# Kernel optimization log

Measured on AMD Instinct MI355X. Metric: run time of the kernel, lower is better.

## Reference

```python
import jax, jax.numpy as jnp
import numpy as np

S, B, QD, VD, E = 2048, 32, 1024, 1024, 1024


def setup_inputs() -> dict:
    key = jax.random.key(0)
    ks = jax.random.split(key, 8)
    query = jax.random.normal(ks[0], (B, QD), dtype=jnp.float32)
    value = jax.random.normal(ks[1], (S, B, VD), dtype=jnp.float32)
    key_padding_mask = jnp.zeros((S, B), dtype=bool)
    # learned params, init as in reset_parameters()
    Wq = jax.random.uniform(ks[2], (E, QD), minval=-0.1, maxval=0.1, dtype=jnp.float32)
    Wv = jax.random.uniform(ks[3], (E, VD), minval=-0.1, maxval=0.1, dtype=jnp.float32)
    v = jax.random.uniform(ks[4], (E,), minval=-0.1, maxval=0.1, dtype=jnp.float32)
    b = jnp.zeros((E,), dtype=jnp.float32)
    g = jnp.full((1,), float(np.sqrt(1.0 / E)), dtype=jnp.float32)
    return {"query": query, "value": value, "Wq": Wq, "Wv": Wv, "v": v, "b": b, "g": g,
            "key_padding_mask": key_padding_mask}


def reference(query, value, Wq, Wv, v, b, g, key_padding_mask):
    # projected_query: (B, E) -> broadcast over seq dim
    pq = query @ Wq.T
    # key: (S, B, E)
    key = jnp.einsum('sbd,ed->sbe', value, Wv)
    normed_v = g * v / jnp.linalg.norm(v)  # (E,)
    # additive (Bahdanau) scores: (S, B)
    attn_scores = jnp.einsum('e,sbe->sb', normed_v, jnp.tanh(pq[None, :, :] + key + b))
    attn_scores = jnp.where(key_padding_mask, -jnp.inf, attn_scores)
    attn_scores = jax.nn.softmax(attn_scores, axis=0)  # softmax over seq dim
    context = jnp.einsum('sb,sbd->bd', attn_scores, value)  # (B, VD)
    return (context, attn_scores, attn_scores)
```

## Files before the change

kernel.cpp:

```cpp
#include <hip/hip_runtime.h>
#include <hip/hip_bf16.h>
#include <stdint.h>

#define SEQ 2048
#define BAT 32
#define EDIM 1024
#define MROWS (SEQ*BAT)

typedef __bf16 bf16x8 __attribute__((ext_vector_type(8)));
typedef float f32x4 __attribute__((ext_vector_type(4)));
typedef unsigned short u16x8 __attribute__((ext_vector_type(8)));

typedef __attribute__((address_space(3))) unsigned int lds_uint;
typedef const __attribute__((address_space(1))) unsigned int glb_uint;

__device__ __forceinline__ void async16(void* lds, const void* g) {
  __builtin_amdgcn_global_load_lds((glb_uint*)g, (lds_uint*)lds, 16, 0, 0);
}

__device__ __forceinline__ unsigned short f2bf(float f) {
  unsigned u = __builtin_bit_cast(unsigned, f);
  u = (u + 0x7FFFu + ((u >> 16) & 1u)) >> 16;
  return (unsigned short)u;
}
__device__ __forceinline__ float bf2f(unsigned short h) {
  return __builtin_bit_cast(float, (unsigned)h << 16);
}

__device__ __forceinline__ float fast_tanh(float x) {
  float xc = fminf(fmaxf(x, -9.f), 9.f);
  float e = __expf(2.f * xc);
  return (e - 1.f) * __builtin_amdgcn_rcpf(e + 1.f);
}

__global__ void k_nv(const float* __restrict__ v, const float* __restrict__ g,
                     float* __restrict__ nv) {
  __shared__ float red[256];
  int t = threadIdx.x;
  float s = 0.f;
  for (int i = t; i < EDIM; i += 256) { float x = v[i]; s += x * x; }
  red[t] = s; __syncthreads();
  for (int o = 128; o > 0; o >>= 1) {
    if (t < o) red[t] += red[t + o];
    __syncthreads();
  }
  float scale = g[0] / sqrtf(red[0]);
  for (int i = t; i < EDIM; i += 256) nv[i] = v[i] * scale;
}

__global__ void k_pqb(const float* __restrict__ query, const float* __restrict__ Wq,
                      const float* __restrict__ bias, float* __restrict__ pqb) {
  __shared__ float wq[1024];
  int e = blockIdx.x;
  int t = threadIdx.x;
  reinterpret_cast<float4*>(wq)[t] =
      reinterpret_cast<const float4*>(Wq + (size_t)e * EDIM)[t];
  __syncthreads();
  int w = t >> 6, lane = t & 63;
  float be = bias[e];
  for (int bb = 0; bb < 8; ++bb) {
    int b_ = w * 8 + bb;
    const float4* q4 = reinterpret_cast<const float4*>(query + (size_t)b_ * EDIM) + lane * 4;
    const float4* w4 = reinterpret_cast<const float4*>(wq) + lane * 4;
    float s = 0.f;
#pragma unroll
    for (int j = 0; j < 4; ++j) {
      float4 a = q4[j], c = w4[j];
      s += a.x * c.x + a.y * c.y + a.z * c.z + a.w * c.w;
    }
#pragma unroll
    for (int m = 32; m > 0; m >>= 1) s += __shfl_xor(s, m);
    if (lane == 0) pqb[(size_t)b_ * EDIM + e] = s + be;
  }
}

__global__ void k_cvt(const float* __restrict__ in, unsigned short* __restrict__ out,
                      long long n8) {
  long long i = (long long)blockIdx.x * blockDim.x + threadIdx.x;
  long long stride = (long long)gridDim.x * blockDim.x;
  for (; i < n8; i += stride) {
    const float4* p = reinterpret_cast<const float4*>(in + i * 8);
    float4 a = p[0], b = p[1];
    u16x8 r;
    r[0] = f2bf(a.x); r[1] = f2bf(a.y); r[2] = f2bf(a.z); r[3] = f2bf(a.w);
    r[4] = f2bf(b.x); r[5] = f2bf(b.y); r[6] = f2bf(b.z); r[7] = f2bf(b.w);
    *reinterpret_cast<u16x8*>(out + i * 8) = r;
  }
}

__global__ __launch_bounds__(512, 1) void k_gemm(
    const unsigned short* __restrict__ A,
    const unsigned short* __restrict__ Bm,
    const float* __restrict__ pqb,
    const float* __restrict__ nv,
    float* __restrict__ part)
{
  __shared__ char smem[2 * 65536 + 4 * 256 * 4];

  const int tid = threadIdx.x;
  const int lane = tid & 63;
  const int wid = tid >> 6;
  const int wm = wid >> 2;
  const int wn = wid & 3;

  const int bid = blockIdx.x;
  const int x = bid & 7;
  const int j = bid >> 3;
  const int mi_blk = x * 32 + (j >> 2);
  const int ni_blk = j & 3;
  const size_t m0 = (size_t)mi_blk * 256;
  const int n0 = ni_blk * 256;

  float* partLds = (float*)(smem + 131072);

  f32x4 acc[8][4];
#pragma unroll
  for (int i = 0; i < 8; ++i)
#pragma unroll
    for (int jj = 0; jj < 4; ++jj) acc[i][jj] = f32x4{0.f, 0.f, 0.f, 0.f};

  const int cs0 = (lane >> 4) ^ (lane & 7);
  const int cs1 = cs0 ^ 4;
  const int rA = lane & 15;

  auto stageA = [&](int slot, int k0) {
#pragma unroll
    for (int i = 0; i < 4; ++i) {
      int chunk = i * 512 + tid;
      int row = chunk >> 3;
      int csrc = (chunk & 7) ^ (row & 7);
      async16(smem + slot * 65536 + chunk * 16,
              A + (m0 + (size_t)row) * 1024 + k0 + csrc * 8);
    }
  };
  auto stageB = [&](int slot, int k0) {
#pragma unroll
    for (int i = 0; i < 4; ++i) {
      int chunk = i * 512 + tid;
      int row = chunk >> 3;
      int csrc = (chunk & 7) ^ (row & 7);
      async16(smem + slot * 65536 + 32768 + chunk * 16,
              Bm + (size_t)(n0 + row) * 1024 + k0 + csrc * 8);
    }
  };

  stageA(0, 0);
  stageB(0, 0);
  __syncthreads();

#pragma unroll 1
  for (int t = 0; t < 16; ++t) {
    char* cb = smem + (t & 1) * 65536;
    const int nslot = (t + 1) & 1;
    const int nk0 = (t + 1) * 64;
    const bool pf = (t + 1) < 16;

    if (pf) stageA(nslot, nk0);

#pragma unroll
    for (int kk = 0; kk < 2; ++kk) {
      const int cs = kk ? cs1 : cs0;
      bf16x8 af[8], bf[4];
#pragma unroll
      for (int mi = 0; mi < 8; ++mi)
        af[mi] = *reinterpret_cast<const bf16x8*>(
            cb + (wm * 128 + mi * 16 + rA) * 128 + cs * 16);
#pragma unroll
      for (int nj = 0; nj < 2; ++nj)
        bf[nj] = *reinterpret_cast<const bf16x8*>(
            cb + 32768 + (wn * 64 + nj * 16 + rA) * 128 + cs * 16);

      __builtin_amdgcn_s_setprio(1);
#pragma unroll
      for (int mi = 0; mi < 8; ++mi)
#pragma unroll
        for (int nj = 0; nj < 2; ++nj)
          acc[mi][nj] = __builtin_amdgcn_mfma_f32_16x16x32_bf16(af[mi], bf[nj], acc[mi][nj], 0, 0, 0);
      __builtin_amdgcn_s_setprio(0);

      if (kk == 0 && pf) stageB(nslot, nk0);

#pragma unroll
      for (int nj = 2; nj < 4; ++nj)
        bf[nj] = *reinterpret_cast<const bf16x8*>(
            cb + 32768 + (wn * 64 + nj * 16 + rA) * 128 + cs * 16);

      __builtin_amdgcn_s_setprio(1);
#pragma unroll
      for (int mi = 0; mi < 8; ++mi)
#pragma unroll
        for (int nj = 2; nj < 4; ++nj)
          acc[mi][nj] = __builtin_amdgcn_mfma_f32_16x16x32_bf16(af[mi], bf[nj], acc[mi][nj], 0, 0, 0);
      __builtin_amdgcn_s_setprio(0);
    }
    __syncthreads();
  }

  const int cgrp = lane >> 4;
  const int ccol = lane & 15;
  float nve[4];
#pragma unroll
  for (int nj = 0; nj < 4; ++nj) nve[nj] = nv[n0 + wn * 64 + nj * 16 + ccol];

#pragma unroll
  for (int mi = 0; mi < 8; ++mi) {
#pragma unroll
    for (int r = 0; r < 4; ++r) {
      int rloc = wm * 128 + mi * 16 + cgrp * 4 + r;
      int b_ = rloc & 31;
      const float* pq = pqb + (size_t)b_ * EDIM + n0 + wn * 64 + ccol;
      float s = 0.f;
#pragma unroll
      for (int nj = 0; nj < 4; ++nj)
        s += nve[nj] * fast_tanh(acc[mi][nj][r] + pq[nj * 16]);
      s += __shfl_xor(s, 1);
      s += __shfl_xor(s, 2);
      s += __shfl_xor(s, 4);
      s += __shfl_xor(s, 8);
      if (ccol == 0) partLds[wn * 256 + rloc] = s;
    }
  }
  __syncthreads();
  if (tid < 256)
    part[(size_t)ni_blk * MROWS + m0 + tid] =
        partLds[tid] + partLds[256 + tid] + partLds[512 + tid] + partLds[768 + tid];
}

__global__ void k_softmax(const float* __restrict__ part,
                          const unsigned char* __restrict__ mask,
                          float* __restrict__ scores,
                          float* __restrict__ out_attn)
{
  int b_ = blockIdx.x;
  int t = threadIdx.x;
  __shared__ float red[256];
  float sc[8];
  float mx = -1e30f;
#pragma unroll
  for (int i = 0; i < 8; ++i) {
    int s_ = t + i * 256;
    size_t r = (size_t)s_ * BAT + b_;
    float v = 0.f;
#pragma unroll
    for (int c = 0; c < 4; ++c) v += part[(size_t)c * MROWS + r];
    if (mask[r]) v = -1e30f;
    sc[i] = v;
    mx = fmaxf(mx, v);
  }
  red[t] = mx; __syncthreads();
  for (int o = 128; o > 0; o >>= 1) {
    if (t < o) red[t] = fmaxf(red[t], red[t + o]);
    __syncthreads();
  }
  mx = red[0];
  __syncthreads();
  float sum = 0.f;
#pragma unroll
  for (int i = 0; i < 8; ++i) { sc[i] = expf(sc[i] - mx); sum += sc[i]; }
  red[t] = sum; __syncthreads();
  for (int o = 128; o > 0; o >>= 1) {
    if (t < o) red[t] += red[t + o];
    __syncthreads();
  }
  float inv = 1.f / red[0];
#pragma unroll
  for (int i = 0; i < 8; ++i) {
    int s_ = t + i * 256;
    size_t r = (size_t)s_ * BAT + b_;
    float w = sc[i] * inv;
    scores[r] = w;
    out_attn[r] = w;
    out_attn[MROWS + r] = w;
  }
}

__global__ void k_ctx(const unsigned short* __restrict__ Vb,
                      const float* __restrict__ scores,
                      float* __restrict__ pctx)
{
  int b_ = blockIdx.x;
  int sch = blockIdx.y;
  int t = threadIdx.x;
  int d8 = t & 127;
  int sr = t >> 7;
  float acc[8];
#pragma unroll
  for (int j = 0; j < 8; ++j) acc[j] = 0.f;
  int s0 = sch * 256;
  for (int i = 0; i < 128; ++i) {
    int s_ = s0 + i * 2 + sr;
    size_t r = (size_t)s_ * BAT + b_;
    float w = scores[r];
    u16x8 v = *reinterpret_cast<const u16x8*>(Vb + r * 1024 + d8 * 8);
#pragma unroll
    for (int j = 0; j < 8; ++j) acc[j] += w * bf2f(v[j]);
  }
  float* dst = pctx + ((size_t)(sch * 2 + sr) * BAT + b_) * 1024 + d8 * 8;
#pragma unroll
  for (int j = 0; j < 8; ++j) dst[j] = acc[j];
}

__global__ void k_ctx_reduce(const float* __restrict__ pctx, float* __restrict__ out) {
  int i = blockIdx.x * 256 + threadIdx.x;
  float s = 0.f;
#pragma unroll
  for (int c = 0; c < 16; ++c) s += pctx[(size_t)c * 32768 + i];
  out[i] = s;
}

extern "C" void kernel_launch(void* const* d_in, const int* in_sizes, int n_in,
                              void* d_out, int out_size, void* d_ws, size_t ws_size,
                              hipStream_t stream) {
  const float* query = (const float*)d_in[0];
  const float* value = (const float*)d_in[1];
  const float* Wq    = (const float*)d_in[2];
  const float* Wv    = (const float*)d_in[3];
  const float* v     = (const float*)d_in[4];
  const float* bias  = (const float*)d_in[5];
  const float* g     = (const float*)d_in[6];
  const unsigned char* mask = (const unsigned char*)d_in[7];
  float* out = (float*)d_out;

  char* ws = (char*)d_ws;
  unsigned short* Vb  = (unsigned short*)ws;
  unsigned short* Wvb = (unsigned short*)(ws + (size_t)134217728);
  float* pqb    = (float*)(ws + (size_t)134217728 + 2097152);
  float* nv     = pqb + 32 * 1024;
  float* part   = nv + 1024;
  float* scores = part + 4 * MROWS;
  float* pctx   = scores + MROWS;

  k_nv<<<1, 256, 0, stream>>>(v, g, nv);
  k_pqb<<<1024, 256, 0, stream>>>(query, Wq, bias, pqb);
  k_cvt<<<2048, 256, 0, stream>>>(value, Vb, (long long)(65536LL * 1024 / 8));
  k_cvt<<<512, 256, 0, stream>>>(Wv, Wvb, (long long)(1024LL * 1024 / 8));
  k_gemm<<<1024, 512, 0, stream>>>(Vb, Wvb, pqb, nv, part);
  k_softmax<<<32, 256, 0, stream>>>(part, mask, scores, out + 32768);
  dim3 gf(32, 8);
  k_ctx<<<gf, 256, 0, stream>>>(Vb, scores, pctx);
  k_ctx_reduce<<<128, 256, 0, stream>>>(pctx, out);
}
```

Before: 273.7 us.

## Switch GEMM to 32x32x16 MFMA with precomputed pointers and unrolled double buffer

Replaces the 16x16x32 bf16 MFMA tiling with 32x32x16 MFMA, so each wave issues 8 larger MFMAs per k-step instead of 32 small ones and needs fewer LDS fragment reads per flop. Global-load addresses are precomputed once and bumped each iteration, and the double-buffer loop is manually unrolled by two to drop per-iteration slot arithmetic. The epilogue is rewritten for the 32x32 accumulator layout with an extra shuffle step. This risks different register pressure and a changed LDS bank-conflict pattern under the new swizzle.

```diff
diff --git a/kernel.cpp b/kernel.cpp
--- a/kernel.cpp
+++ b/kernel.cpp
@@ -8,7 +8,7 @@
 #define MROWS (SEQ*BAT)
 
 typedef __bf16 bf16x8 __attribute__((ext_vector_type(8)));
-typedef float f32x4 __attribute__((ext_vector_type(4)));
+typedef float f32x16 __attribute__((ext_vector_type(16)));
 typedef unsigned short u16x8 __attribute__((ext_vector_type(8)));
 
 typedef __attribute__((address_space(3))) unsigned int lds_uint;
@@ -102,122 +102,116 @@
   const int wid = tid >> 6;
   const int wm = wid >> 2;
   const int wn = wid & 3;
+  const int l31 = lane & 31;
+  const int hi = lane >> 5;
 
   const int bid = blockIdx.x;
-  const int x = bid & 7;
+  const int xcd = bid & 7;
   const int j = bid >> 3;
-  const int mi_blk = x * 32 + (j >> 2);
+  const int mi_blk = xcd * 32 + (j >> 2);
   const int ni_blk = j & 3;
   const size_t m0 = (size_t)mi_blk * 256;
   const int n0 = ni_blk * 256;
 
   float* partLds = (float*)(smem + 131072);
 
-  f32x4 acc[8][4];
-#pragma unroll
-  for (int i = 0; i < 8; ++i)
-#pragma unroll
-    for (int jj = 0; jj < 4; ++jj) acc[i][jj] = f32x4{0.f, 0.f, 0.f, 0.f};
-
-  const int cs0 = (lane >> 4) ^ (lane & 7);
-  const int cs1 = cs0 ^ 4;
-  const int rA = lane & 15;
-
-  auto stageA = [&](int slot, int k0) {
-#pragma unroll
-    for (int i = 0; i < 4; ++i) {
-      int chunk = i * 512 + tid;
-      int row = chunk >> 3;
-      int csrc = (chunk & 7) ^ (row & 7);
-      async16(smem + slot * 65536 + chunk * 16,
-              A + (m0 + (size_t)row) * 1024 + k0 + csrc * 8);
-    }
+  f32x16 acc[4][2];
+#pragma unroll
+  for (int i = 0; i < 4; ++i)
+#pragma unroll
+    for (int jj = 0; jj < 2; ++jj) acc[i][jj] = (f32x16)(0.f);
+
+  const int csrc = (tid & 7) ^ ((tid >> 3) & 7);
+  const unsigned short* gA[4];
+  const unsigned short* gB[4];
+#pragma unroll
+  for (int i = 0; i < 4; ++i) {
+    int row = i * 64 + (tid >> 3);
+    gA[i] = A + (m0 + (size_t)row) * 1024 + csrc * 8;
+    gB[i] = Bm + (size_t)(n0 + row) * 1024 + csrc * 8;
+  }
+  const int ldsOffA = tid * 16;
+  const int ldsOffB = 32768 + tid * 16;
+
+  const int swz = ((hi ^ (lane & 7)) << 4);
+  const int rdA = (wm * 128 + l31) * 128 + swz;
+  const int rdB = 32768 + (wn * 64 + l31) * 128 + swz;
+
+  auto stageA = [&](char* sl) {
+#pragma unroll
+    for (int i = 0; i < 4; ++i)
+      async16(sl + ldsOffA + i * 8192, gA[i]);
   };
-  auto stageB = [&](int slot, int k0) {
-#pragma unroll
-    for (int i = 0; i < 4; ++i) {
-      int chunk = i * 512 + tid;
-      int row = chunk >> 3;
-      int csrc = (chunk & 7) ^ (row & 7);
-      async16(smem + slot * 65536 + 32768 + chunk * 16,
-              Bm + (size_t)(n0 + row) * 1024 + k0 + csrc * 8);
-    }
+  auto stageB = [&](char* sl) {
+#pragma unroll
+    for (int i = 0; i < 4; ++i)
+      async16(sl + ldsOffB + i * 8192, gB[i]);
   };
-
-  stageA(0, 0);
-  stageB(0, 0);
+  auto bump = [&]() {
+#pragma unroll
+    for (int i = 0; i < 4; ++i) { gA[i] += 64; gB[i] += 64; }
+  };
+
+  char* buf0 = smem;
+  char* buf1 = smem + 65536;
+
+  stageA(buf0);
+  stageB(buf0);
+  bump();
   __syncthreads();
 
-#pragma unroll 1
-  for (int t = 0; t < 16; ++t) {
-    char* cb = smem + (t & 1) * 65536;
-    const int nslot = (t + 1) & 1;
-    const int nk0 = (t + 1) * 64;
-    const bool pf = (t + 1) < 16;
-
-    if (pf) stageA(nslot, nk0);
-
-#pragma unroll
-    for (int kk = 0; kk < 2; ++kk) {
-      const int cs = kk ? cs1 : cs0;
-      bf16x8 af[8], bf[4];
-#pragma unroll
-      for (int mi = 0; mi < 8; ++mi)
-        af[mi] = *reinterpret_cast<const bf16x8*>(
-            cb + (wm * 128 + mi * 16 + rA) * 128 + cs * 16);
-#pragma unroll
-      for (int nj = 0; nj < 2; ++nj)
-        bf[nj] = *reinterpret_cast<const bf16x8*>(
-            cb + 32768 + (wn * 64 + nj * 16 + rA) * 128 + cs * 16);
+  auto body = [&](char* cb, char* nb, bool pf) {
+    if (pf) stageA(nb);
+#pragma unroll
+    for (int ks = 0; ks < 4; ++ks) {
+      const int x = ks << 5;
+      bf16x8 af[4], bf[2];
+#pragma unroll
+      for (int fm = 0; fm < 4; ++fm)
+        af[fm] = *reinterpret_cast<const bf16x8*>(cb + ((rdA ^ x) + fm * 4096));
+#pragma unroll
+      for (int fn = 0; fn < 2; ++fn)
+        bf[fn] = *reinterpret_cast<const bf16x8*>(cb + ((rdB ^ x) + fn * 4096));
+
+      if (ks == 1 && pf) stageB(nb);
 
       __builtin_amdgcn_s_setprio(1);
 #pragma unroll
-      for (int mi = 0; mi < 8; ++mi)
-#pragma unroll
-        for (int nj = 0; nj < 2; ++nj)
-          acc[mi][nj] = __builtin_amdgcn_mfma_f32_16x16x32_bf16(af[mi], bf[nj], acc[mi][nj], 0, 0, 0);
-      __builtin_amdgcn_s_setprio(0);
-
-      if (kk == 0 && pf) stageB(nslot, nk0);
-
-#pragma unroll
-      for (int nj = 2; nj < 4; ++nj)
-        bf[nj] = *reinterpret_cast<const bf16x8*>(
-            cb + 32768 + (wn * 64 + nj * 16 + rA) * 128 + cs * 16);
-
-      __builtin_amdgcn_s_setprio(1);
-#pragma unroll
-      for (int mi = 0; mi < 8; ++mi)
-#pragma unroll
-        for (int nj = 2; nj < 4; ++nj)
-          acc[mi][nj] = __builtin_amdgcn_mfma_f32_16x16x32_bf16(af[mi], bf[nj], acc[mi][nj], 0, 0, 0);
+      for (int fm = 0; fm < 4; ++fm)
+#pragma unroll
+        for (int fn = 0; fn < 2; ++fn)
+          acc[fm][fn] = __builtin_amdgcn_mfma_f32_32x32x16_bf16(af[fm], bf[fn], acc[fm][fn], 0, 0, 0);
       __builtin_amdgcn_s_setprio(0);
     }
+    if (pf) bump();
     __syncthreads();
-  }
-
-  const int cgrp = lane >> 4;
-  const int ccol = lane & 15;
-  float nve[4];
-#pragma unroll
-  for (int nj = 0; nj < 4; ++nj) nve[nj] = nv[n0 + wn * 64 + nj * 16 + ccol];
-
-#pragma unroll
-  for (int mi = 0; mi < 8; ++mi) {
-#pragma unroll
-    for (int r = 0; r < 4; ++r) {
-      int rloc = wm * 128 + mi * 16 + cgrp * 4 + r;
-      int b_ = rloc & 31;
-      const float* pq = pqb + (size_t)b_ * EDIM + n0 + wn * 64 + ccol;
-      float s = 0.f;
-#pragma unroll
-      for (int nj = 0; nj < 4; ++nj)
-        s += nve[nj] * fast_tanh(acc[mi][nj][r] + pq[nj * 16]);
+  };
+
+#pragma unroll 1
+  for (int tt = 0; tt < 8; ++tt) {
+    body(buf0, buf1, true);
+    body(buf1, buf0, tt < 7);
+  }
+
+  float nve[2];
+#pragma unroll
+  for (int fn = 0; fn < 2; ++fn) nve[fn] = nv[n0 + wn * 64 + fn * 32 + l31];
+
+#pragma unroll
+  for (int fm = 0; fm < 4; ++fm) {
+#pragma unroll
+    for (int r = 0; r < 16; ++r) {
+      int b_ = (r & 3) + 8 * (r >> 2) + 4 * hi;
+      int m_loc = wm * 128 + fm * 32 + b_;
+      const float* pq = pqb + (size_t)b_ * EDIM + n0 + wn * 64 + l31;
+      float s = nve[0] * fast_tanh(acc[fm][0][r] + pq[0]) +
+                nve[1] * fast_tanh(acc[fm][1][r] + pq[32]);
       s += __shfl_xor(s, 1);
       s += __shfl_xor(s, 2);
       s += __shfl_xor(s, 4);
       s += __shfl_xor(s, 8);
-      if (ccol == 0) partLds[wn * 256 + rloc] = s;
+      s += __shfl_xor(s, 16);
+      if (l31 == 0) partLds[wn * 256 + m_loc] = s;
     }
   }
   __syncthreads();
```

After: 309.9 us. +13.2%, slower.

## Restructure GEMM mainloop into 4-stage K=32 pipeline with vmcnt waits

Applied to the files above, without the earlier changes.

Replaces the double-buffered K=64 tile loop with a four-slot ring of K=32 tiles, prefetching three stages ahead. Each step uses one barrier plus explicit s_waitcnt vmcnt counts instead of a full __syncthreads after every tile. The LDS swizzle is reworked for 64-byte rows. The aim is to hide global-load latency better and cut synchronisation stalls. In exchange it has twice as many barriers per K, and correctness now depends on hand-picked vmcnt values and buffer reuse ordering.

```diff
diff --git a/kernel.cpp b/kernel.cpp
--- a/kernel.cpp
+++ b/kernel.cpp
@@ -13,6 +13,8 @@
 
 typedef __attribute__((address_space(3))) unsigned int lds_uint;
 typedef const __attribute__((address_space(1))) unsigned int glb_uint;
+
+#define WAITV(n) asm volatile("s_waitcnt vmcnt(" #n ")" ::: "memory")
 
 __device__ __forceinline__ void async16(void* lds, const void* g) {
   __builtin_amdgcn_global_load_lds((glb_uint*)g, (lds_uint*)lds, 16, 0, 0);
@@ -95,7 +97,7 @@
     const float* __restrict__ nv,
     float* __restrict__ part)
 {
-  __shared__ char smem[2 * 65536 + 4 * 256 * 4];
+  __shared__ char smem[4 * 32768 + 4 * 256 * 4];
 
   const int tid = threadIdx.x;
   const int lane = tid & 63;
@@ -104,9 +106,9 @@
   const int wn = wid & 3;
 
   const int bid = blockIdx.x;
-  const int x = bid & 7;
+  const int xcd = bid & 7;
   const int j = bid >> 3;
-  const int mi_blk = x * 32 + (j >> 2);
+  const int mi_blk = xcd * 32 + (j >> 2);
   const int ni_blk = j & 3;
   const size_t m0 = (size_t)mi_blk * 256;
   const int n0 = ni_blk * 256;
@@ -119,88 +121,70 @@
 #pragma unroll
     for (int jj = 0; jj < 4; ++jj) acc[i][jj] = f32x4{0.f, 0.f, 0.f, 0.f};
 
-  const int cs0 = (lane >> 4) ^ (lane & 7);
-  const int cs1 = cs0 ^ 4;
+  const int csrc = (tid & 3) ^ ((tid >> 2) & 3);
+  const int row0 = tid >> 2;
+  const unsigned short* gA0 = A + (m0 + (size_t)row0) * 1024 + csrc * 8;
+  const unsigned short* gA1 = gA0 + 128 * 1024;
+  const unsigned short* gB0 = Bm + (size_t)(n0 + row0) * 1024 + csrc * 8;
+  const unsigned short* gB1 = gB0 + 128 * 1024;
+  const int dst0 = tid * 16;
+
+  auto stage = [&](char* buf) {
+    async16(buf + dst0, gA0);
+    async16(buf + 8192 + dst0, gA1);
+    async16(buf + 16384 + dst0, gB0);
+    async16(buf + 24576 + dst0, gB1);
+    gA0 += 32; gA1 += 32; gB0 += 32; gB1 += 32;
+  };
+
   const int rA = lane & 15;
-
-  auto stageA = [&](int slot, int k0) {
-#pragma unroll
-    for (int i = 0; i < 4; ++i) {
-      int chunk = i * 512 + tid;
-      int row = chunk >> 3;
-      int csrc = (chunk & 7) ^ (row & 7);
-      async16(smem + slot * 65536 + chunk * 16,
-              A + (m0 + (size_t)row) * 1024 + k0 + csrc * 8);
-    }
+  const int swz = (((lane >> 4) ^ (lane & 3)) << 4);
+  const int rdA = (wm * 128 + rA) * 64 + swz;
+  const int rdB = 16384 + (wn * 64 + rA) * 64 + swz;
+
+  auto half_step = [&](char* cb, char* sb) {
+    __builtin_amdgcn_s_barrier();
+    if (sb) stage(sb);
+    bf16x8 af[8], bf[4];
+#pragma unroll
+    for (int mi = 0; mi < 8; ++mi)
+      af[mi] = *reinterpret_cast<const bf16x8*>(cb + rdA + mi * 1024);
+#pragma unroll
+    for (int fn = 0; fn < 4; ++fn)
+      bf[fn] = *reinterpret_cast<const bf16x8*>(cb + rdB + fn * 1024);
+    __builtin_amdgcn_s_setprio(1);
+#pragma unroll
+    for (int mi = 0; mi < 8; ++mi)
+#pragma unroll
+      for (int fn = 0; fn < 4; ++fn)
+        acc[mi][fn] = __builtin_amdgcn_mfma_f32_16x16x32_bf16(af[mi], bf[fn], acc[mi][fn], 0, 0, 0);
+    __builtin_amdgcn_s_setprio(0);
   };
-  auto stageB = [&](int slot, int k0) {
-#pragma unroll
-    for (int i = 0; i < 4; ++i) {
-      int chunk = i * 512 + tid;
-      int row = chunk >> 3;
-      int csrc = (chunk & 7) ^ (row & 7);
-      async16(smem + slot * 65536 + 32768 + chunk * 16,
-              Bm + (size_t)(n0 + row) * 1024 + k0 + csrc * 8);
-    }
-  };
-
-  stageA(0, 0);
-  stageB(0, 0);
-  __syncthreads();
+
+  char* b0 = smem;
+  char* b1 = smem + 32768;
+  char* b2 = smem + 65536;
+  char* b3 = smem + 98304;
+
+  stage(b0); stage(b1); stage(b2);
 
 #pragma unroll 1
-  for (int t = 0; t < 16; ++t) {
-    char* cb = smem + (t & 1) * 65536;
-    const int nslot = (t + 1) & 1;
-    const int nk0 = (t + 1) * 64;
-    const bool pf = (t + 1) < 16;
-
-    if (pf) stageA(nslot, nk0);
-
-#pragma unroll
-    for (int kk = 0; kk < 2; ++kk) {
-      const int cs = kk ? cs1 : cs0;
-      bf16x8 af[8], bf[4];
-#pragma unroll
-      for (int mi = 0; mi < 8; ++mi)
-        af[mi] = *reinterpret_cast<const bf16x8*>(
-            cb + (wm * 128 + mi * 16 + rA) * 128 + cs * 16);
-#pragma unroll
-      for (int nj = 0; nj < 2; ++nj)
-        bf[nj] = *reinterpret_cast<const bf16x8*>(
-            cb + 32768 + (wn * 64 + nj * 16 + rA) * 128 + cs * 16);
-
-      __builtin_amdgcn_s_setprio(1);
-#pragma unroll
-      for (int mi = 0; mi < 8; ++mi)
-#pragma unroll
-        for (int nj = 0; nj < 2; ++nj)
-          acc[mi][nj] = __builtin_amdgcn_mfma_f32_16x16x32_bf16(af[mi], bf[nj], acc[mi][nj], 0, 0, 0);
-      __builtin_amdgcn_s_setprio(0);
-
-      if (kk == 0 && pf) stageB(nslot, nk0);
-
-#pragma unroll
-      for (int nj = 2; nj < 4; ++nj)
-        bf[nj] = *reinterpret_cast<const bf16x8*>(
-            cb + 32768 + (wn * 64 + nj * 16 + rA) * 128 + cs * 16);
-
-      __builtin_amdgcn_s_setprio(1);
-#pragma unroll
-      for (int mi = 0; mi < 8; ++mi)
-#pragma unroll
-        for (int nj = 2; nj < 4; ++nj)
-          acc[mi][nj] = __builtin_amdgcn_mfma_f32_16x16x32_bf16(af[mi], bf[nj], acc[mi][nj], 0, 0, 0);
-      __builtin_amdgcn_s_setprio(0);
-    }
-    __syncthreads();
-  }
+  for (int it = 0; it < 7; ++it) {
+    WAITV(8); half_step(b0, b3);
+    WAITV(8); half_step(b1, b0);
+    WAITV(8); half_step(b2, b1);
+    WAITV(8); half_step(b3, b2);
+  }
+  WAITV(8); half_step(b0, b3);
+  WAITV(8); half_step(b1, nullptr);
+  WAITV(4); half_step(b2, nullptr);
+  WAITV(0); half_step(b3, nullptr);
 
   const int cgrp = lane >> 4;
   const int ccol = lane & 15;
   float nve[4];
 #pragma unroll
-  for (int nj = 0; nj < 4; ++nj) nve[nj] = nv[n0 + wn * 64 + nj * 16 + ccol];
+  for (int fn = 0; fn < 4; ++fn) nve[fn] = nv[n0 + wn * 64 + fn * 16 + ccol];
 
 #pragma unroll
   for (int mi = 0; mi < 8; ++mi) {
@@ -211,8 +195,8 @@
       const float* pq = pqb + (size_t)b_ * EDIM + n0 + wn * 64 + ccol;
       float s = 0.f;
 #pragma unroll
-      for (int nj = 0; nj < 4; ++nj)
-        s += nve[nj] * fast_tanh(acc[mi][nj][r] + pq[nj * 16]);
+      for (int fn = 0; fn < 4; ++fn)
+        s += nve[fn] * fast_tanh(acc[mi][fn][r] + pq[fn * 16]);
       s += __shfl_xor(s, 1);
       s += __shfl_xor(s, 2);
       s += __shfl_xor(s, 4);
```

New measurement: 286.4 us. 4.6% more time.

## Fuse fp32-to-bf16 conversion of value into GEMM A-tile loading

Applied to the files above, without the earlier changes.

Removes the separate conversion kernel over the large value tensor. The GEMM now loads fp32 value rows into registers, converts them to bf16 and writes them to LDS. Blocks in the first N-tile column also write the bf16 copy to global memory for the later context kernel. This saves one full read and write pass of the 256MB tensor, but each of the four N-blocks per row tile now reads the fp32 A data (twice the bytes of bf16) instead of using async global-to-LDS loads, which adds register pressure and synchronous load latency. Conversion also switches to the compiler's native bf16 cast instead of manual rounding.

```diff
diff --git a/kernel.cpp b/kernel.cpp
--- a/kernel.cpp
+++ b/kernel.cpp
@@ -25,6 +25,13 @@
 }
 __device__ __forceinline__ float bf2f(unsigned short h) {
   return __builtin_bit_cast(float, (unsigned)h << 16);
+}
+
+__device__ __forceinline__ u16x8 cvt8(float4 a, float4 b) {
+  bf16x8 r;
+  r[0] = (__bf16)a.x; r[1] = (__bf16)a.y; r[2] = (__bf16)a.z; r[3] = (__bf16)a.w;
+  r[4] = (__bf16)b.x; r[5] = (__bf16)b.y; r[6] = (__bf16)b.z; r[7] = (__bf16)b.w;
+  return __builtin_bit_cast(u16x8, r);
 }
 
 __device__ __forceinline__ float fast_tanh(float x) {
@@ -81,18 +88,16 @@
   for (; i < n8; i += stride) {
     const float4* p = reinterpret_cast<const float4*>(in + i * 8);
     float4 a = p[0], b = p[1];
-    u16x8 r;
-    r[0] = f2bf(a.x); r[1] = f2bf(a.y); r[2] = f2bf(a.z); r[3] = f2bf(a.w);
-    r[4] = f2bf(b.x); r[5] = f2bf(b.y); r[6] = f2bf(b.z); r[7] = f2bf(b.w);
-    *reinterpret_cast<u16x8*>(out + i * 8) = r;
+    *reinterpret_cast<u16x8*>(out + i * 8) = cvt8(a, b);
   }
 }
 
 __global__ __launch_bounds__(512, 1) void k_gemm(
-    const unsigned short* __restrict__ A,
+    const float* __restrict__ value,
     const unsigned short* __restrict__ Bm,
     const float* __restrict__ pqb,
     const float* __restrict__ nv,
+    unsigned short* __restrict__ Vb,
     float* __restrict__ part)
 {
   __shared__ char smem[2 * 65536 + 4 * 256 * 4];
@@ -104,12 +109,13 @@
   const int wn = wid & 3;
 
   const int bid = blockIdx.x;
-  const int x = bid & 7;
+  const int xcd = bid & 7;
   const int j = bid >> 3;
-  const int mi_blk = x * 32 + (j >> 2);
+  const int mi_blk = xcd * 32 + (j >> 2);
   const int ni_blk = j & 3;
   const size_t m0 = (size_t)mi_blk * 256;
   const int n0 = ni_blk * 256;
+  const bool doVb = (ni_blk == 0);
 
   float* partLds = (float*)(smem + 131072);
 
@@ -119,44 +125,66 @@
 #pragma unroll
     for (int jj = 0; jj < 4; ++jj) acc[i][jj] = f32x4{0.f, 0.f, 0.f, 0.f};
 
+  const int csrc = (tid & 7) ^ ((tid >> 3) & 7);
+  const int rowt = tid >> 3;
+  const float* gvA[4];
+  unsigned short* vbo[4];
+#pragma unroll
+  for (int i = 0; i < 4; ++i) {
+    size_t row = m0 + (size_t)(i * 64 + rowt);
+    gvA[i] = value + row * 1024 + (tid & 7) * 8;
+    vbo[i] = Vb + row * 1024 + (tid & 7) * 8;
+  }
+  const int dstA0 = rowt * 128 + csrc * 16;
+  float4 ar[8];
+
+  auto loadA = [&]() {
+#pragma unroll
+    for (int i = 0; i < 4; ++i) {
+      ar[2 * i]     = *reinterpret_cast<const float4*>(gvA[i]);
+      ar[2 * i + 1] = *reinterpret_cast<const float4*>(gvA[i] + 4);
+    }
+  };
+  auto writeA = [&](char* nb) {
+#pragma unroll
+    for (int i = 0; i < 4; ++i) {
+      u16x8 c = cvt8(ar[2 * i], ar[2 * i + 1]);
+      *reinterpret_cast<u16x8*>(nb + i * 8192 + dstA0) = c;
+      if (doVb) *reinterpret_cast<u16x8*>(vbo[i]) = c;
+      gvA[i] += 64;
+      vbo[i] += 64;
+    }
+  };
+
+  const unsigned short* gB[4];
+#pragma unroll
+  for (int i = 0; i < 4; ++i) {
+    int row = i * 64 + rowt;
+    gB[i] = Bm + (size_t)(n0 + row) * 1024 + csrc * 8;
+  }
+  const int ldsOffB = 32768 + tid * 16;
+  auto stageB = [&](char* sl) {
+#pragma unroll
+    for (int i = 0; i < 4; ++i) {
+      async16(sl + ldsOffB + i * 8192, gB[i]);
+      gB[i] += 64;
+    }
+  };
+
+  const int rA = lane & 15;
   const int cs0 = (lane >> 4) ^ (lane & 7);
   const int cs1 = cs0 ^ 4;
-  const int rA = lane & 15;
-
-  auto stageA = [&](int slot, int k0) {
-#pragma unroll
-    for (int i = 0; i < 4; ++i) {
-      int chunk = i * 512 + tid;
-      int row = chunk >> 3;
-      int csrc = (chunk & 7) ^ (row & 7);
-      async16(smem + slot * 65536 + chunk * 16,
-              A + (m0 + (size_t)row) * 1024 + k0 + csrc * 8);
-    }
-  };
-  auto stageB = [&](int slot, int k0) {
-#pragma unroll
-    for (int i = 0; i < 4; ++i) {
-      int chunk = i * 512 + tid;
-      int row = chunk >> 3;
-      int csrc = (chunk & 7) ^ (row & 7);
-      async16(smem + slot * 65536 + 32768 + chunk * 16,
-              Bm + (size_t)(n0 + row) * 1024 + k0 + csrc * 8);
-    }
-  };
-
-  stageA(0, 0);
-  stageB(0, 0);
+
+  char* buf0 = smem;
+  char* buf1 = smem + 65536;
+
+  loadA();
+  stageB(buf0);
+  writeA(buf0);
   __syncthreads();
 
-#pragma unroll 1
-  for (int t = 0; t < 16; ++t) {
-    char* cb = smem + (t & 1) * 65536;
-    const int nslot = (t + 1) & 1;
-    const int nk0 = (t + 1) * 64;
-    const bool pf = (t + 1) < 16;
-
-    if (pf) stageA(nslot, nk0);
-
+  auto body = [&](char* cb, char* nb, bool pf) {
+    if (pf) loadA();
 #pragma unroll
     for (int kk = 0; kk < 2; ++kk) {
       const int cs = kk ? cs1 : cs0;
@@ -178,7 +206,7 @@
           acc[mi][nj] = __builtin_amdgcn_mfma_f32_16x16x32_bf16(af[mi], bf[nj], acc[mi][nj], 0, 0, 0);
       __builtin_amdgcn_s_setprio(0);
 
-      if (kk == 0 && pf) stageB(nslot, nk0);
+      if (kk == 0 && pf) stageB(nb);
 
 #pragma unroll
       for (int nj = 2; nj < 4; ++nj)
@@ -193,7 +221,14 @@
           acc[mi][nj] = __builtin_amdgcn_mfma_f32_16x16x32_bf16(af[mi], bf[nj], acc[mi][nj], 0, 0, 0);
       __builtin_amdgcn_s_setprio(0);
     }
+    if (pf) writeA(nb);
     __syncthreads();
+  };
+
+#pragma unroll 1
+  for (int tt = 0; tt < 8; ++tt) {
+    body(buf0, buf1, true);
+    body(buf1, buf0, tt < 7);
   }
 
   const int cgrp = lane >> 4;
@@ -332,9 +367,8 @@
 
   k_nv<<<1, 256, 0, stream>>>(v, g, nv);
   k_pqb<<<1024, 256, 0, stream>>>(query, Wq, bias, pqb);
-  k_cvt<<<2048, 256, 0, stream>>>(value, Vb, (long long)(65536LL * 1024 / 8));
   k_cvt<<<512, 256, 0, stream>>>(Wv, Wvb, (long long)(1024LL * 1024 / 8));
-  k_gemm<<<1024, 512, 0, stream>>>(Vb, Wvb, pqb, nv, part);
+  k_gemm<<<1024, 512, 0, stream>>>(value, Wvb, pqb, nv, Vb, part);
   k_softmax<<<32, 256, 0, stream>>>(part, mask, scores, out + 32768);
   dim3 gf(32, 8);
   k_ctx<<<gf, 256, 0, stream>>>(Vb, scores, pctx);
```

Measured after the change: 416.6 us. 1.52x slower.
